# Kernel optimization log

Hardware: AMD Instinct MI355X
Metric: run time of the kernel (lower is better)

The kernel has to match this reference:

```python
import jax, jax.numpy as jnp
import numpy as np

B, N, C = 2, 2048, 768
H = 12
D = C // H
SCALE = D ** -0.5
EPS = 1e-5
HID = 4 * C


def layer_norm(x, g, b):
    mu = jnp.mean(x, axis=-1, keepdims=True)
    var = jnp.var(x, axis=-1, keepdims=True)
    return (x - mu) * jax.lax.rsqrt(var + EPS) * g + b


def setup_inputs():
    key = jax.random.key(0)
    ks = jax.random.split(key, 12)
    s = C ** -0.5
    x = jax.random.normal(ks[0], (B, N, C), dtype=jnp.float32)
    mask = (jax.random.uniform(ks[1], (B, N, N)) < 0.1).astype(jnp.float32)
    return {
        "x": x,
        "mask": mask,
        "g1": jnp.ones((C,), jnp.float32),
        "b1": jnp.zeros((C,), jnp.float32),
        "Wq": jax.random.normal(ks[2], (C, C), jnp.float32) * s,
        "Wkv": jax.random.normal(ks[3], (2 * C, C), jnp.float32) * s,
        "Wp": jax.random.normal(ks[4], (C, C), jnp.float32) * s,
        "bp": jnp.zeros((C,), jnp.float32),
        "g2": jnp.ones((C,), jnp.float32),
        "b2": jnp.zeros((C,), jnp.float32),
        "W1": jax.random.normal(ks[5], (HID, C), jnp.float32) * s,
        "bf1": jnp.zeros((HID,), jnp.float32),
        "W2": jax.random.normal(ks[6], (C, HID), jnp.float32) * (HID ** -0.5),
        "bf2": jnpmp if False else jnp.zeros((C,), jnp.float32),
    }


def block_fwd(x, mask, g1, b1, Wq, Wkv, Wp, bp, g2, b2, W1, bf1, W2, bf2):
    # --- attention branch (pre-norm) ---
    xn = layer_norm(x, g1, b1)
    q = (xn @ Wq.T).reshape(B, N, H, D).transpose(0, 2, 1, 3)      # bhnd
    kv = (xn @ Wkv.T).reshape(B, N, 2, H, D).transpose(2, 0, 3, 1, 4)
    k, v = kv[0], kv[1]                                             # bhnd
    attn = jnp.einsum('bhnd,bhmd->bhnm', q, k) * SCALE
    attn = attn + (mask * -100000.0)[:, None]                       # additive mask
    attn = jax.nn.softmax(attn, axis=-1)
    o = jnp.einsum('bhnm,bhmd->bhnd', attn, v)
    o = o.transpose(0, 2, 1, 3).reshape(B, N, C)
    o = o @ Wp.T + bp
    x = x + o
    # --- MLP branch (pre-norm) ---
    xn2 = layer_norm(x, g2, b2)
    h = jax.nn.gelu(xn2 @ W1.T + bf1, approximate=False)
    x = x + (h @ W2.T + bf2)
    return x


def reference(x, mask, g1, b1, Wq, Wkv, Wp, bp, g2, b2, W1, bf1, W2, bf2):
    return block_fwd(x, mask, g1, b1, Wq, Wkv, Wp, bp, g2, b2, W1, bf1, W2, bf2)
```

## Files before the change

kernel.cpp:

```cpp
#include <hip/hip_runtime.h>
#include <hip/hip_bf16.h>
#include <cstdint>
#include <cstddef>

#define BB 2
#define NN 2048
#define CC 768
#define HH 12
#define DD 64
#define HID 3072
#define TT (BB*NN)

typedef __attribute__((ext_vector_type(8))) short bf16x8;
typedef __attribute__((ext_vector_type(4))) short bf16x4;
typedef __attribute__((ext_vector_type(4))) float f32x4;

__device__ __forceinline__ unsigned short f2bf(float f) {
    unsigned int u = __float_as_uint(f);
    u += 0x7fffu + ((u >> 16) & 1u);
    return (unsigned short)(u >> 16);
}
__device__ __forceinline__ float bf2f(unsigned short u) {
    return __uint_as_float(((unsigned int)u) << 16);
}
#if __has_builtin(__builtin_amdgcn_exp2f)
#define EXP2F(x) __builtin_amdgcn_exp2f(x)
#else
#define EXP2F(x) exp2f(x)
#endif

__device__ __forceinline__ void gload16(const void* g, void* l) {
    __builtin_amdgcn_global_load_lds((__attribute__((address_space(1))) unsigned int*)g,
                                     (__attribute__((address_space(3))) unsigned int*)l,
                                     16, 0, 0);
}

#define WAITV(N) asm volatile("s_waitcnt vmcnt(" #N ")" ::: "memory")
#define WAITLGKM asm volatile("s_waitcnt lgkmcnt(0)" ::: "memory")

typedef __attribute__((ext_vector_type(4))) float float4v;
typedef __attribute__((ext_vector_type(4))) unsigned short ushort4v;

struct PrepArgs {
    const float* x; const float* g1; const float* b1; unsigned short* xn;
    const float* cin[5]; unsigned short* cout[5]; int n4[5];
    const float* mask; unsigned short* mb;
};
__global__ __launch_bounds__(256) void prep_kernel(PrepArgs a) {
    int id = blockIdx.x;
    int tid = threadIdx.x;
    if (id < TT) {
        const float* xr = a.x + (size_t)id * CC;
        float v0 = xr[tid], v1 = xr[tid + 256], v2 = xr[tid + 512];
        float s = v0 + v1 + v2;
        float s2 = v0 * v0 + v1 * v1 + v2 * v2;
#pragma unroll
        for (int off = 1; off < 64; off <<= 1) {
            s  += __shfl_xor(s, off);
            s2 += __shfl_xor(s2, off);
        }
        __shared__ float red[8];
        int wv = tid >> 6, lane = tid & 63;
        if (lane == 0) { red[wv] = s; red[wv + 4] = s2; }
        __syncthreads();
        s  = red[0] + red[1] + red[2] + red[3];
        s2 = red[4] + red[5] + red[6] + red[7];
        float mu   = s * (1.0f / CC);
        float var  = s2 * (1.0f / CC) - mu * mu;
        float rstd = rsqrtf(var + 1e-5f);
        unsigned short* orow = a.xn + (size_t)id * CC;
        orow[tid]       = f2bf((v0 - mu) * rstd * a.g1[tid]       + a.b1[tid]);
        orow[tid + 256] = f2bf((v1 - mu) * rstd * a.g1[tid + 256] + a.b1[tid + 256]);
        orow[tid + 512] = f2bf((v2 - mu) * rstd * a.g1[tid + 512] + a.b1[tid + 512]);
    } else if (id < TT + 1024) {
        int base = (id - TT) * 256 + tid;
        int stride = 1024 * 256;
#pragma unroll
        for (int sseg = 0; sseg < 5; ++sseg) {
            const float4v* ip = (const float4v*)a.cin[sseg];
            ushort4v* op = (ushort4v*)a.cout[sseg];
            for (int i = base; i < a.n4[sseg]; i += stride) {
                float4v v = ip[i];
                ushort4v o;
                o[0] = f2bf(v[0]); o[1] = f2bf(v[1]); o[2] = f2bf(v[2]); o[3] = f2bf(v[3]);
                op[i] = o;
            }
        }
    } else {
        int base = (id - TT - 1024) * 256 + tid;
        int stride = 1024 * 256;
        int n = BB * NN * (NN / 16);
        for (int i = base; i < n; i += stride) {
            const float4v* mp = (const float4v*)(a.mask + (size_t)i * 16);
            unsigned int bits = 0;
#pragma unroll
            for (int q = 0; q < 4; ++q) {
                float4v v = mp[q];
#pragma unroll
                for (int j = 0; j < 4; ++j) bits |= (v[j] > 0.5f) ? (1u << (q * 4 + j)) : 0u;
            }
            a.mb[i] = (unsigned short)bits;
        }
    }
}

__global__ __launch_bounds__(256) void ln_kernel(const float* __restrict__ x,
                                                 const float* __restrict__ g,
                                                 const float* __restrict__ b,
                                                 unsigned short* __restrict__ out) {
    int t = blockIdx.x;
    int tid = threadIdx.x;
    const float* xr = x + (size_t)t * CC;
    float v0 = xr[tid], v1 = xr[tid + 256], v2 = xr[tid + 512];
    float s = v0 + v1 + v2;
    float s2 = v0 * v0 + v1 * v1 + v2 * v2;
#pragma unroll
    for (int off = 1; off < 64; off <<= 1) {
        s  += __shfl_xor(s, off);
        s2 += __shfl_xor(s2, off);
    }
    __shared__ float red[8];
    int wv = tid >> 6, lane = tid & 63;
    if (lane == 0) { red[wv] = s; red[wv + 4] = s2; }
    __syncthreads();
    s  = red[0] + red[1] + red[2] + red[3];
    s2 = red[4] + red[5] + red[6] + red[7];
    float mu   = s * (1.0f / CC);
    float var  = s2 * (1.0f / CC) - mu * mu;
    float rstd = rsqrtf(var + 1e-5f);
    unsigned short* orow = out + (size_t)t * CC;
    orow[tid]       = f2bf((v0 - mu) * rstd * g[tid]       + b[tid]);
    orow[tid + 256] = f2bf((v1 - mu) * rstd * g[tid + 256] + b[tid + 256]);
    orow[tid + 512] = f2bf((v2 - mu) * rstd * g[tid + 512] + b[tid + 512]);
}

template <int EPI, int BM>
__global__ __launch_bounds__(256) void gemm_bt(const unsigned short* __restrict__ A,
                                               const unsigned short* __restrict__ Bw,
                                               const float* __restrict__ bias,
                                               const float* __restrict__ res,
                                               void* __restrict__ out,
                                               int M, int N, int K) {
    constexpr int MI = BM / 32;
    constexpr int NCA = (BM * 4) / 256;
    __shared__ alignas(16) unsigned short As[2][BM * 32];
    __shared__ alignas(16) unsigned short Bs[2][128 * 32];
    int tid = threadIdx.x;
    int lane = tid & 63, wv = tid >> 6;
    int l16 = lane & 15, lg = lane >> 4;
    int bm = blockIdx.x, bn = blockIdx.y;
    int wm = (wv & 1) * (BM / 2), wn = (wv >> 1) * 64;

    const unsigned short* Ab = A + (size_t)bm * BM * K;
    const unsigned short* Bb = Bw + (size_t)bn * 128 * K;

    const unsigned short* aSrc[NCA]; int aDst[NCA];
#pragma unroll
    for (int i = 0; i < NCA; ++i) {
        int c = tid + i * 256;
        int row = c >> 2, p = c & 3;
        int lc = p ^ ((row >> 1) & 3);
        aSrc[i] = Ab + (size_t)row * K + lc * 8;
        aDst[i] = c * 8;
    }
    const unsigned short* bSrc[2]; int bDst[2];
#pragma unroll
    for (int i = 0; i < 2; ++i) {
        int c = tid + i * 256;
        int row = c >> 2, p = c & 3;
        int lc = p ^ ((row >> 1) & 3);
        bSrc[i] = Bb + (size_t)row * K + lc * 8;
        bDst[i] = c * 8;
    }
    int aoff = (wm + l16) * 32 + ((lg ^ (((wm + l16) >> 1) & 3)) * 8);
    int boff = (wn + l16) * 32 + ((lg ^ (((wn + l16) >> 1) & 3)) * 8);

    f32x4 acc[MI][4];
#pragma unroll
    for (int i = 0; i < MI; ++i)
#pragma unroll
        for (int j = 0; j < 4; ++j) acc[i][j] = f32x4{0.f, 0.f, 0.f, 0.f};

    auto STAGE = [&](int s, int k0) {
#pragma unroll
        for (int i = 0; i < NCA; ++i) gload16(aSrc[i] + k0, &As[s][aDst[i]]);
#pragma unroll
        for (int i = 0; i < 2; ++i)   gload16(bSrc[i] + k0, &Bs[s][bDst[i]]);
    };

    STAGE(0, 0);
    int nt = K / 32;
    for (int t = 0; t < nt; ++t) {
        int cur = t & 1;
        if (t + 1 < nt) {
            STAGE(cur ^ 1, (t + 1) * 32);
            if constexpr (NCA + 2 == 4) { WAITV(4); } else { WAITV(3); }
        } else {
            WAITV(0);
        }
        __builtin_amdgcn_s_barrier();
        bf16x8 af[MI], bfr[4];
#pragma unroll
        for (int mi = 0; mi < MI; ++mi) af[mi]  = *(const bf16x8*)&As[cur][aoff + mi * 512];
#pragma unroll
        for (int ni = 0; ni < 4; ++ni)  bfr[ni] = *(const bf16x8*)&Bs[cur][boff + ni * 512];
#pragma unroll
        for (int mi = 0; mi < MI; ++mi)
#pragma unroll
            for (int ni = 0; ni < 4; ++ni)
                acc[mi][ni] = __builtin_amdgcn_mfma_f32_16x16x32_bf16(bfr[ni], af[mi], acc[mi][ni], 0, 0, 0);
        WAITLGKM;
        __builtin_amdgcn_s_barrier();
    }

#pragma unroll
    for (int mi = 0; mi < MI; ++mi) {
        int row = bm * BM + wm + mi * 16 + l16;
#pragma unroll
        for (int ni = 0; ni < 4; ++ni) {
            int col = bn * 128 + wn + ni * 16 + lg * 4;
            size_t idx = (size_t)row * N + col;
            f32x4 v = acc[mi][ni];
            if (EPI == 0) {
                bf16x4 ov;
#pragma unroll
                for (int r2 = 0; r2 < 4; ++r2) ov[r2] = (short)f2bf(v[r2]);
                *(bf16x4*)((unsigned short*)out + idx) = ov;
            } else if (EPI == 1 || EPI == 3) {
                f32x4 bv = *(const f32x4*)&bias[col];
                f32x4 rv = *(const f32x4*)&res[idx];
                f32x4 ov;
#pragma unroll
                for (int r2 = 0; r2 < 4; ++r2) ov[r2] = v[r2] + bv[r2] + rv[r2];
                *(f32x4*)((float*)out + idx) = ov;
            } else {
                f32x4 bv = *(const f32x4*)&bias[col];
                bf16x4 ov;
#pragma unroll
                for (int r2 = 0; r2 < 4; ++r2) {
                    float t2 = v[r2] + bv[r2];
                    t2 = 0.5f * t2 * (1.0f + erff(t2 * 0.70710678118f));
                    ov[r2] = (short)f2bf(t2);
                }
                *(bf16x4*)((unsigned short*)out + idx) = ov;
            }
        }
    }
}

#define KVB 64
#define ANT (NN/KVB)
#define VP 68
__global__ __launch_bounds__(256) void attn_kernel(const unsigned short* __restrict__ qkv,
                                                   const unsigned short* __restrict__ maskb,
                                                   unsigned short* __restrict__ o) {
    __shared__ alignas(16) unsigned short Ks[2][64 * 64];
    __shared__ alignas(16) unsigned short Vt[2][64 * VP];
    int tid = threadIdx.x;
    int lane = tid & 63, wv = tid >> 6;
    int l16 = lane & 15, lg = lane >> 4;
    int id = blockIdx.x;
    int xcd = id & 7, r = id >> 3;
    int bh = xcd * 3 + (r % 3);
    int qb = r / 3;
    int b = bh / HH, h = bh % HH;
    int qrow = qb * 64 + wv * 16 + l16;

    const unsigned short* qp = qkv + ((size_t)(b * NN + qrow)) * 2304 + h * DD;
    bf16x8 q0r = *(const bf16x8*)(qp + 8 * lg);
    bf16x8 q1r = *(const bf16x8*)(qp + 32 + 8 * lg);
    const float QSC = 0.125f * 1.4426950408889634f;
    bf16x8 q0, q1;
#pragma unroll
    for (int j = 0; j < 8; ++j) {
        q0[j] = (short)f2bf(bf2f((unsigned short)q0r[j]) * QSC);
        q1[j] = (short)f2bf(bf2f((unsigned short)q1r[j]) * QSC);
    }

    const unsigned short* mrow  = maskb + ((size_t)(b * NN + qrow)) * 128;
    const unsigned short* kbase = qkv + (size_t)b * NN * 2304 + 768 + h * DD;
    const unsigned short* vbase = qkv + (size_t)b * NN * 2304 + 1536 + h * DD;

    const unsigned short* kSrc[2]; int kDst[2];
#pragma unroll
    for (int i = 0; i < 2; ++i) {
        int c = tid + i * 256;
        int row = c >> 3, p = c & 7;
        int lc = p ^ (row & 7);
        kSrc[i] = kbase + (size_t)row * 2304 + lc * 8;
        kDst[i] = c * 8;
    }
    int kp = tid & 31, dg = tid >> 5;
    const unsigned short* vSrc = vbase + (size_t)(2 * kp) * 2304 + dg * 8;

    int sw = l16 & 7;
    int kb0 = l16 * 64 + ((lg ^ sw) * 8);
    int kb1 = l16 * 64 + (((lg + 4) ^ sw) * 8);
    int vbo = l16 * VP + lg * 4;

    bf16x8 va, vb;
    unsigned long long mb_cur, mb_nxt;

    f32x4 oa[4];
#pragma unroll
    for (int i = 0; i < 4; ++i) oa[i] = f32x4{0.f, 0.f, 0.f, 0.f};
    float lrun = 0.f;

    auto LOAD = [&](int t, int s) {
        const unsigned short* vp = vSrc + (size_t)t * KVB * 2304;
        va = *(const bf16x8*)(vp);
        vb = *(const bf16x8*)(vp + 2304);
        mb_nxt = *(const unsigned long long*)(mrow + t * 4);
        __builtin_amdgcn_sched_barrier(0);
#pragma unroll
        for (int i = 0; i < 2; ++i) gload16(kSrc[i] + (size_t)t * KVB * 2304, &Ks[s][kDst[i]]);
    };
    auto WRITEV = [&](int s) {
        unsigned int* VtU = (unsigned int*)Vt[s];
#pragma unroll
        for (int j = 0; j < 8; ++j)
            VtU[(dg * 8 + j) * (VP / 2) + kp] =
                (unsigned int)(unsigned short)va[j] | ((unsigned int)(unsigned short)vb[j] << 16);
    };

    LOAD(0, 0);
    WAITV(2);
    WRITEV(0);
    mb_cur = mb_nxt;
    int cur = 0;

    for (int kt = 0; kt < ANT; ++kt) {
        bool pre = (kt + 1 < ANT);
        WAITV(0);
        WAITLGKM;
        __builtin_amdgcn_s_barrier();
        if (pre) LOAD(kt + 1, cur ^ 1);

        const unsigned short* Ksc = Ks[cur];
        const unsigned short* Vtc = Vt[cur];

        float ps = 0.f;
        bf16x4 pf[4];
#pragma unroll
        for (int ks = 0; ks < 4; ++ks) {
            bf16x8 k0 = *(const bf16x8*)&Ksc[kb0 + ks * 1024];
            bf16x8 k1 = *(const bf16x8*)&Ksc[kb1 + ks * 1024];
            f32x4 sa = f32x4{0.f, 0.f, 0.f, 0.f};
            sa = __builtin_amdgcn_mfma_f32_16x16x32_bf16(k0, q0, sa, 0, 0, 0);
            sa = __builtin_amdgcn_mfma_f32_16x16x32_bf16(k1, q1, sa, 0, 0, 0);
            unsigned int m16 = (unsigned int)(mb_cur >> (ks * 16 + lg * 4));
#pragma unroll
            for (int r2 = 0; r2 < 4; ++r2) {
                float mbit = (float)((m16 >> r2) & 1u);
                float p = EXP2F(fmaf(mbit, -144269.5f, sa[r2]));
                ps += p;
                pf[ks][r2] = (short)(__float_as_uint(p) >> 16);
            }
        }
        lrun += ps;

#pragma unroll
        for (int ks = 0; ks < 4; ++ks)
#pragma unroll
            for (int db = 0; db < 4; ++db) {
                bf16x4 vf = *(const bf16x4*)&Vtc[vbo + db * 16 * VP + ks * 16];
                oa[db] = __builtin_amdgcn_mfma_f32_16x16x16bf16_1k(vf, pf[ks], oa[db], 0, 0, 0);
            }

        if (pre) {
            WAITV(2);
            WRITEV(cur ^ 1);
            cur ^= 1;
            mb_cur = mb_nxt;
        }
    }

    float lt = lrun;
    lt += __shfl_xor(lt, 16);
    lt += __shfl_xor(lt, 32);
    float inv = 1.0f / lt;
    unsigned short* op = o + ((size_t)(b * NN + qrow)) * CC + h * DD;
#pragma unroll
    for (int db = 0; db < 4; ++db) {
        bf16x4 ov;
#pragma unroll
        for (int r2 = 0; r2 < 4; ++r2) ov[r2] = (short)f2bf(oa[db][r2] * inv);
        *(bf16x4*)&op[db * 16 + lg * 4] = ov;
    }
}

extern "C" void kernel_launch(void* const* d_in, const int* in_sizes, int n_in,
                              void* d_out, int out_size, void* d_ws, size_t ws_size,
                              hipStream_t stream) {
    const float* x    = (const float*)d_in[0];
    const float* mask = (const float*)d_in[1];
    const float* g1   = (const float*)d_in[2];
    const float* b1   = (const float*)d_in[3];
    const float* Wq   = (const float*)d_in[4];
    const float* Wkv  = (const float*)d_in[5];
    const float* Wp   = (const float*)d_in[6];
    const float* bp   = (const float*)d_in[7];
    const float* g2   = (const float*)d_in[8];
    const float* b2   = (const float*)d_in[9];
    const float* W1   = (const float*)d_in[10];
    const float* bf1  = (const float*)d_in[11];
    const float* W2   = (const float*)d_in[12];
    const float* bf2  = (const float*)d_in[13];
    float* out = (float*)d_out;

    char* w = (char*)d_ws;
    unsigned short* wqkv = (unsigned short*)w;      w += (size_t)2304 * 768 * 2;
    unsigned short* wp   = (unsigned short*)w;      w += (size_t)768 * 768 * 2;
    unsigned short* w1   = (unsigned short*)w;      w += (size_t)3072 * 768 * 2;
    unsigned short* w2   = (unsigned short*)w;      w += (size_t)768 * 3072 * 2;
    unsigned short* xn   = (unsigned short*)w;      w += (size_t)TT * CC * 2;
    unsigned short* qkv  = (unsigned short*)w;      w += (size_t)TT * 2304 * 2;
    unsigned short* mb   = (unsigned short*)w;      w += (size_t)BB * NN * 128 * 2;
    unsigned short* obuf = (unsigned short*)w;      w += (size_t)TT * CC * 2;
    float*          x1   = (float*)w;               w += (size_t)TT * CC * 4;
    unsigned short* xn2  = (unsigned short*)w;      w += (size_t)TT * CC * 2;
    unsigned short* hbuf = (unsigned short*)w;      w += (size_t)TT * HID * 2;

    PrepArgs pa;
    pa.x = x; pa.g1 = g1; pa.b1 = b1; pa.xn = xn;
    pa.cin[0] = Wq;  pa.cout[0] = wqkv;             pa.n4[0] = 768 * 768 / 4;
    pa.cin[1] = Wkv; pa.cout[1] = wqkv + 768 * 768; pa.n4[1] = 1536 * 768 / 4;
    pa.cin[2] = Wp;  pa.cout[2] = wp;               pa.n4[2] = 768 * 768 / 4;
    pa.cin[3] = W1;  pa.cout[3] = w1;               pa.n4[3] = 3072 * 768 / 4;
    pa.cin[4] = W2;  pa.cout[4] = w2;               pa.n4[4] = 768 * 3072 / 4;
    pa.mask = mask; pa.mb = mb;
    prep_kernel<<<TT + 2048, 256, 0, stream>>>(pa);

    gemm_bt<0, 64><<<dim3(TT / 64, 2304 / 128), 256, 0, stream>>>(xn, wqkv, nullptr, nullptr, qkv, TT, 2304, 768);

    attn_kernel<<<32 * 24, 256, 0, stream>>>(qkv, mb, obuf);

    gemm_bt<1, 64><<<dim3(TT / 64, 768 / 128), 256, 0, stream>>>(obuf, wp, bp, x, x1, TT, 768, 768);

    ln_kernel<<<TT, 256, 0, stream>>>(x1, g2, b2, xn2);

    gemm_bt<2, 64><<<dim3(TT / 64, HID / 128), 256, 0, stream>>>(xn2, w1, bf1, nullptr, hbuf, TT, HID, 768);

    gemm_bt<3, 64><<<dim3(TT / 64, 768 / 128), 256, 0, stream>>>(hbuf, w2, bf2, x1, out, TT, 768, HID);
}
```

Baseline: 228.8 us.

## Split attention KV range across two blocks, combine partials; enlarge GEMM M tiles

The attention kernel now splits each query tile's 2048-key range into two halves handled by separate blocks, doubling the grid. Each block writes unnormalized fp32 partial outputs and row sums, and a new combine kernel adds them, normalizes, and emits bf16. The plain-sum combine is valid only because the kernel exponentiates scores without a running max. The QKV and W1 GEMMs also switch to a 128-row M tile. The split adds fp32 partial traffic and an extra launch, and the partials reuse the hbuf and x1 workspace buffers.

```diff
diff --git a/kernel.cpp b/kernel.cpp
--- a/kernel.cpp
+++ b/kernel.cpp
@@ -14,6 +14,9 @@
 typedef __attribute__((ext_vector_type(8))) short bf16x8;
 typedef __attribute__((ext_vector_type(4))) short bf16x4;
 typedef __attribute__((ext_vector_type(4))) float f32x4;
+typedef __attribute__((ext_vector_type(4))) float float4v;
+typedef __attribute__((ext_vector_type(4))) unsigned short ushort4v;
+typedef __attribute__((ext_vector_type(8))) unsigned short ushort8v;
 
 __device__ __forceinline__ unsigned short f2bf(float f) {
     unsigned int u = __float_as_uint(f);
@@ -37,9 +40,6 @@
 
 #define WAITV(N) asm volatile("s_waitcnt vmcnt(" #N ")" ::: "memory")
 #define WAITLGKM asm volatile("s_waitcnt lgkmcnt(0)" ::: "memory")
-
-typedef __attribute__((ext_vector_type(4))) float float4v;
-typedef __attribute__((ext_vector_type(4))) unsigned short ushort4v;
 
 struct PrepArgs {
     const float* x; const float* g1; const float* b1; unsigned short* xn;
@@ -249,22 +249,26 @@
 }
 
 #define KVB 64
-#define ANT (NN/KVB)
+#define HNT 16
 #define VP 68
 __global__ __launch_bounds__(256) void attn_kernel(const unsigned short* __restrict__ qkv,
                                                    const unsigned short* __restrict__ maskb,
-                                                   unsigned short* __restrict__ o) {
+                                                   float* __restrict__ Op,
+                                                   float* __restrict__ lp) {
     __shared__ alignas(16) unsigned short Ks[2][64 * 64];
     __shared__ alignas(16) unsigned short Vt[2][64 * VP];
     int tid = threadIdx.x;
     int lane = tid & 63, wv = tid >> 6;
     int l16 = lane & 15, lg = lane >> 4;
     int id = blockIdx.x;
-    int xcd = id & 7, r = id >> 3;
+    int half = id & 1;
+    int rid = id >> 1;
+    int xcd = rid & 7, r = rid >> 3;
     int bh = xcd * 3 + (r % 3);
     int qb = r / 3;
     int b = bh / HH, h = bh % HH;
     int qrow = qb * 64 + wv * 16 + l16;
+    int kt0 = half * HNT;
 
     const unsigned short* qp = qkv + ((size_t)(b * NN + qrow)) * 2304 + h * DD;
     bf16x8 q0r = *(const bf16x8*)(qp + 8 * lg);
@@ -323,18 +327,18 @@
                 (unsigned int)(unsigned short)va[j] | ((unsigned int)(unsigned short)vb[j] << 16);
     };
 
-    LOAD(0, 0);
+    LOAD(kt0, 0);
     WAITV(2);
     WRITEV(0);
     mb_cur = mb_nxt;
     int cur = 0;
 
-    for (int kt = 0; kt < ANT; ++kt) {
-        bool pre = (kt + 1 < ANT);
+    for (int t = 0; t < HNT; ++t) {
+        bool pre = (t + 1 < HNT);
         WAITV(0);
         WAITLGKM;
         __builtin_amdgcn_s_barrier();
-        if (pre) LOAD(kt + 1, cur ^ 1);
+        if (pre) LOAD(kt0 + t + 1, cur ^ 1);
 
         const unsigned short* Ksc = Ks[cur];
         const unsigned short* Vtc = Vt[cur];
@@ -378,15 +382,37 @@
     float lt = lrun;
     lt += __shfl_xor(lt, 16);
     lt += __shfl_xor(lt, 32);
-    float inv = 1.0f / lt;
-    unsigned short* op = o + ((size_t)(b * NN + qrow)) * CC + h * DD;
-#pragma unroll
-    for (int db = 0; db < 4; ++db) {
-        bf16x4 ov;
-#pragma unroll
-        for (int r2 = 0; r2 < 4; ++r2) ov[r2] = (short)f2bf(oa[db][r2] * inv);
-        *(bf16x4*)&op[db * 16 + lg * 4] = ov;
-    }
+    lp[(size_t)half * TT * HH + (size_t)(b * NN + qrow) * HH + h] = lt;
+
+    float* opf = Op + (size_t)half * TT * CC + (size_t)(b * NN + qrow) * CC + h * DD;
+#pragma unroll
+    for (int db = 0; db < 4; ++db)
+        *(f32x4*)&opf[db * 16 + lg * 4] = oa[db];
+}
+
+__global__ __launch_bounds__(256) void combine_kernel(const float* __restrict__ Op,
+                                                      const float* __restrict__ lp,
+                                                      unsigned short* __restrict__ obuf) {
+    int i8 = blockIdx.x * 256 + threadIdx.x;
+    size_t i = (size_t)i8 * 8;
+    int token = i8 / 96;
+    int c8 = i8 % 96;
+    int h = c8 >> 3;
+    size_t lidx = (size_t)token * HH + h;
+    float ls = lp[lidx] + lp[(size_t)TT * HH + lidx];
+    float inv = 1.0f / ls;
+    const float* O0 = Op;
+    const float* O1 = Op + (size_t)TT * CC;
+    f32x4 a0 = *(const f32x4*)&O0[i];
+    f32x4 a1 = *(const f32x4*)&O0[i + 4];
+    f32x4 b0 = *(const f32x4*)&O1[i];
+    f32x4 b1 = *(const f32x4*)&O1[i + 4];
+    ushort8v o;
+#pragma unroll
+    for (int j = 0; j < 4; ++j) o[j]     = f2bf((a0[j] + b0[j]) * inv);
+#pragma unroll
+    for (int j = 0; j < 4; ++j) o[4 + j] = f2bf((a1[j] + b1[j]) * inv);
+    *(ushort8v*)&obuf[i] = o;
 }
 
 extern "C" void kernel_launch(void* const* d_in, const int* in_sizes, int n_in,
@@ -421,6 +447,9 @@
     unsigned short* xn2  = (unsigned short*)w;      w += (size_t)TT * CC * 2;
     unsigned short* hbuf = (unsigned short*)w;      w += (size_t)TT * HID * 2;
 
+    float* Op = (float*)hbuf;
+    float* lp = (float*)x1;
+
     PrepArgs pa;
     pa.x = x; pa.g1 = g1; pa.b1 = b1; pa.xn = xn;
     pa.cin[0] = Wq;  pa.cout[0] = wqkv;             pa.n4[0] = 768 * 768 / 4;
@@ -431,15 +460,16 @@
     pa.mask = mask; pa.mb = mb;
     prep_kernel<<<TT + 2048, 256, 0, stream>>>(pa);
 
-    gemm_bt<0, 64><<<dim3(TT / 64, 2304 / 128), 256, 0, stream>>>(xn, wqkv, nullptr, nullptr, qkv, TT, 2304, 768);
-
-    attn_kernel<<<32 * 24, 256, 0, stream>>>(qkv, mb, obuf);
+    gemm_bt<0, 128><<<dim3(TT / 128, 2304 / 128), 256, 0, stream>>>(xn, wqkv, nullptr, nullptr, qkv, TT, 2304, 768);
+
+    attn_kernel<<<1536, 256, 0, stream>>>(qkv, mb, Op, lp);
+    combine_kernel<<<TT * CC / 8 / 256, 256, 0, stream>>>(Op, lp, obuf);
 
     gemm_bt<1, 64><<<dim3(TT / 64, 768 / 128), 256, 0, stream>>>(obuf, wp, bp, x, x1, TT, 768, 768);
 
     ln_kernel<<<TT, 256, 0, stream>>>(x1, g2, b2, xn2);
 
-    gemm_bt<2, 64><<<dim3(TT / 64, HID / 128), 256, 0, stream>>>(xn2, w1, bf1, nullptr, hbuf, TT, HID, 768);
+    gemm_bt<2, 128><<<dim3(TT / 128, HID / 128), 256, 0, stream>>>(xn2, w1, bf1, nullptr, hbuf, TT, HID, 768);
 
     gemm_bt<3, 64><<<dim3(TT / 64, 768 / 128), 256, 0, stream>>>(hbuf, w2, bf2, x1, out, TT, 768, HID);
 }
```

Result: faster. 218.7 us (-4.4%).
